# Kernel tuning notes

Hardware: AMD Instinct MI355X
Metric: run time of the kernel (lower is better)

The kernel has to match this reference:

```python
import jax, jax.numpy as jnp
import numpy as np
import math

B, H, L, S, D = 16, 10, 4096, 77, 64
N_EMB = 20            # subject tokens per instance (positions 4..23)
SHRINK = 2.0          # subj_attn_var_shrink_factor


def setup_inputs() -> dict:
    key = jax.random.key(0)
    kq, kk, kv = jax.random.split(key, 3)
    query = jax.random.normal(kq, (B, H, L, D), dtype=jnp.float32)
    k = jax.random.normal(kk, (B, H, S, D), dtype=jnp.float32)
    v = jax.random.normal(kv, (B, H, S, D), dtype=jnp.float32)
    # instance-major subject indices: every batch instance owns tokens 4..23
    idx_b = jnp.repeat(jnp.arange(B, dtype=jnp.int32), N_EMB).reshape(B, N_EMB)
    idx_n = jnp.tile(jnp.arange(4, 4 + N_EMB, dtype=jnp.int32), (B, 1))
    return {"query": query, "key": k, "value": v, "idx_b": idx_b, "idx_n": idx_n}


def _subj_attn_scales(attn_score, idx_b, idx_n, shrink_factor):
    # attn_score: [B,H,L,S] -> permute to [B,S,H,L] as in torch code
    a2 = jnp.transpose(attn_score, (0, 3, 1, 2))
    # gather subject-token attention: [N_SUB, N_EMB, H, L]
    subj = a2[idx_b, idx_n]
    n_sub, n_emb = subj.shape[0], subj.shape[1]
    subj = subj.mean(axis=2)                       # mean over heads -> [NS,NE,L]
    prob = jax.nn.softmax(subj, axis=2)            # over spatial positions
    Hs = Ws = int(math.isqrt(L))
    p3 = prob.reshape(n_sub, n_emb, Hs, Ws)        # [NS,NE,H,W]
    ys = jnp.arange(Hs, dtype=p3.dtype).reshape(1, 1, Hs, 1)
    xs = jnp.arange(Ws, dtype=p3.dtype).reshape(1, 1, 1, Ws)
    y_c = (p3 * ys).sum(axis=(2, 3))               # [NS,NE]
    x_c = (p3 * xs).sum(axis=(2, 3))
    var_y = (p3 * ys ** 2).sum(axis=(2, 3)) - y_c ** 2
    var_x = (p3 * xs ** 2).sum(axis=(2, 3)) - x_c ** 2
    s_x = jnp.sqrt(var_x) / (shrink_factor - 1.0)
    s_y = jnp.sqrt(var_y) / (shrink_factor - 1.0)
    # torch.meshgrid default is 'ij'
    X, Y = jnp.meshgrid(jnp.arange(Ws, dtype=p3.dtype), jnp.arange(Hs, dtype=p3.dtype), indexing="ij")
    X = X[:, :, None, None]
    Y = Y[:, :, None, None]
    grid = jnp.exp(-((X - x_c) ** 2 / (2 * s_x ** 2) + (Y - y_c) ** 2 / (2 * s_y ** 2)))  # [W,H,NS,NE]
    grid = grid / jax.lax.stop_gradient(grid.max())
    grid = jnp.transpose(grid, (2, 3, 0, 1)).reshape(n_sub, n_emb, 1, L)
    # scatter back into ones: [B,S,1,L]
    scales = jnp.ones((B, S, 1, L), dtype=attn_score.dtype)
    scales = scales.at[idx_b, idx_n].set(grid)
    return jnp.transpose(scales, (0, 2, 3, 1))     # [B,1,L,S]


def reference(query, key, value, idx_b, idx_n):
    scale = 1.0 / math.sqrt(query.shape[-1])
    attn_score = jnp.einsum("bhld,bhsd->bhls", query, key) * scale  # [B,H,L,S]
    scales = _subj_attn_scales(attn_score, idx_b, idx_n, SHRINK)
    attn_w = jax.nn.softmax(attn_score, axis=-1) * scales
    out = jnp.einsum("bhls,bhsd->bhld", attn_w, value)              # [B,H,L,D]
    return out
```

## Files before the change

### kernel.cpp

```cpp
#include <hip/hip_runtime.h>
#include <math.h>

#define B_ 16
#define H_ 10
#define L_ 4096
#define S_ 77
#define D_ 64
#define NE_ 20
#define NP_ (B_*NE_)
#define SHRINK_ 2.0f
#define LOG2E 1.4426950408889634f
#define SC_L2 (0.125f*LOG2E)
#define IT_ 8

typedef __bf16 bf16x8 __attribute__((ext_vector_type(8)));
typedef float  f32x4  __attribute__((ext_vector_type(4)));

static __device__ __forceinline__ unsigned short bfb(__bf16 x) {
  return __builtin_bit_cast(unsigned short, x);
}
static __device__ __forceinline__ __bf16 mkbf(unsigned short x) {
  return __builtin_bit_cast(__bf16, x);
}

__global__ __launch_bounds__(256, 3) void k1_subj(const float* __restrict__ Q,
                                                  const float* __restrict__ K,
                                                  const int* __restrict__ idxb,
                                                  const int* __restrict__ idxn,
                                                  float* __restrict__ subj) {
  __shared__ __bf16 KF[20][2][64][8];
  __shared__ float T[NE_][66];
  __shared__ int bs[NE_], ss[NE_], s_uni;
  const int i = blockIdx.y, bx = blockIdx.x;
  const int tid = threadIdx.x, lane = tid & 63, wid = tid >> 6;
  const int c = lane & 15, g = lane >> 4;
  if (tid < NE_) { bs[tid] = idxb[i*NE_ + tid]; ss[tid] = idxn[i*NE_ + tid]; }
  __syncthreads();
  if (tid == 0) { int u = 1; for (int j = 1; j < NE_; ++j) u &= (bs[j] == bs[0]); s_uni = u; }
  for (int e4 = tid; e4 < 32*160; e4 += 256) {
    int j = e4 / 160, k = (e4 - j*160) * 4;
    float4 kv = make_float4(0.f, 0.f, 0.f, 0.f);
    if (j < NE_) kv = *(const float4*)&K[(((size_t)bs[j]*H_ + (k >> 6))*S_ + ss[j])*D_ + (k & 63)];
    int ks = k >> 5, gg = (k >> 3) & 3, jj = k & 7, n = j >> 4, cc = j & 15;
    uint2 pk;
    pk.x = (unsigned)bfb((__bf16)kv.x) | ((unsigned)bfb((__bf16)kv.y) << 16);
    pk.y = (unsigned)bfb((__bf16)kv.z) | ((unsigned)bfb((__bf16)kv.w) << 16);
    *(uint2*)&KF[ks][n][gg*16 + cc][jj] = pk;
  }
  __syncthreads();
  if (!s_uni) {
    int ll = tid & 63;
    for (int ii = 0; ii < 2; ++ii) {
      int l = bx*128 + ii*64 + ll;
      for (int j = tid >> 6; j < NE_; j += 4) {
        float a = 0.f;
        for (int h = 0; h < H_; ++h) {
          const float* qp = Q + (((size_t)bs[j]*H_ + h)*L_ + l)*D_;
          const float* kp = K + (((size_t)bs[j]*H_ + h)*S_ + ss[j])*D_;
          for (int d = 0; d < 64; ++d) a += qp[d]*kp[d];
        }
        subj[(size_t)(i*NE_ + j)*L_ + l] = a * (1.0f/80.0f);
      }
    }
    return;
  }
  const int b0 = bs[0];
  #pragma unroll 1
  for (int it = 0; it < 2; ++it) {
    const int lrow = bx*128 + it*64 + wid*16 + c;
    f32x4 acc0 = {0.f,0.f,0.f,0.f}, acc1 = {0.f,0.f,0.f,0.f};
    #pragma unroll 4
    for (int ks = 0; ks < 20; ++ks) {
      const float* qp = Q + (((size_t)b0*H_ + (ks >> 1))*L_ + lrow)*D_ + (ks & 1)*32 + g*8;
      const float4 a = *(const float4*)qp;
      const float4 bq = *(const float4*)(qp + 4);
      bf16x8 af;
      af[0]=(__bf16)a.x;  af[1]=(__bf16)a.y;  af[2]=(__bf16)a.z;  af[3]=(__bf16)a.w;
      af[4]=(__bf16)bq.x; af[5]=(__bf16)bq.y; af[6]=(__bf16)bq.z; af[7]=(__bf16)bq.w;
      bf16x8 k0 = *(bf16x8*)&KF[ks][0][lane][0];
      bf16x8 k1 = *(bf16x8*)&KF[ks][1][lane][0];
      acc0 = __builtin_amdgcn_mfma_f32_16x16x32_bf16(af, k0, acc0, 0, 0, 0);
      acc1 = __builtin_amdgcn_mfma_f32_16x16x32_bf16(af, k1, acc1, 0, 0, 0);
    }
    const float sc = 1.0f/80.0f;
    #pragma unroll
    for (int r = 0; r < 4; ++r) {
      int ll = wid*16 + g*4 + r;
      T[c][ll] = acc0[r]*sc;
      if (c < 4) T[16 + c][ll] = acc1[r]*sc;
    }
    __syncthreads();
    for (int e = tid; e < NE_*64; e += 256) {
      int j = e >> 6, ll = e & 63;
      subj[(size_t)(i*NE_ + j)*L_ + bx*128 + it*64 + ll] = T[j][ll];
    }
    __syncthreads();
  }
}

__global__ __launch_bounds__(256) void k2_moments(const float* __restrict__ subj,
                                                  float* __restrict__ params) {
  const int p = blockIdx.x;
  const int tid = threadIdx.x;
  const int lane = tid & 63, wid = tid >> 6;
  const float* sp = subj + (size_t)p*L_;
  __shared__ float red[4];
  float m = -1e30f;
  for (int l = tid; l < L_; l += 256) m = fmaxf(m, sp[l]);
  #pragma unroll
  for (int s = 1; s < 64; s <<= 1) m = fmaxf(m, __shfl_xor(m, s, 64));
  if (lane == 0) red[wid] = m;
  __syncthreads();
  m = fmaxf(fmaxf(red[0], red[1]), fmaxf(red[2], red[3]));
  __syncthreads();
  float se = 0, sy = 0, sx = 0, syy = 0, sxx = 0;
  for (int l = tid; l < L_; l += 256) {
    float e = __expf(sp[l] - m);
    float y = (float)(l >> 6), x = (float)(l & 63);
    se += e; sy += e*y; sx += e*x; syy += e*y*y; sxx += e*x*x;
  }
  float vals[5] = {se, sy, sx, syy, sxx};
  #pragma unroll
  for (int q = 0; q < 5; ++q) {
    float v = vals[q];
    #pragma unroll
    for (int s = 1; s < 64; s <<= 1) v += __shfl_xor(v, s, 64);
    if (lane == 0) red[wid] = v;
    __syncthreads();
    v = red[0] + red[1] + red[2] + red[3];
    __syncthreads();
    vals[q] = v;
  }
  if (tid == 0) {
    float xc = vals[2]/vals[0], yc = vals[1]/vals[0];
    float varx = vals[4]/vals[0] - xc*xc;
    float vary = vals[3]/vals[0] - yc*yc;
    float sh = SHRINK_ - 1.0f;
    float isx = sh*sh/(2.f*varx), isy = sh*sh/(2.f*vary);
    float rx = rintf(xc), ry = rintf(yc);
    float mv = __expf(-((rx-xc)*(rx-xc)*isx + (ry-yc)*(ry-yc)*isy));
    params[p*8+0] = xc; params[p*8+1] = yc;
    params[p*8+2] = isx; params[p*8+3] = isy; params[p*8+4] = mv;
  }
}

__global__ __launch_bounds__(256) void k2b_finish(const float* __restrict__ params,
                                                  const int* __restrict__ idxb,
                                                  const int* __restrict__ idxn,
                                                  int* __restrict__ pmap,
                                                  float* __restrict__ l2invg) {
  const int tid = threadIdx.x;
  for (int e = tid; e < B_*S_; e += 256) pmap[e] = -1;
  __syncthreads();
  for (int p = tid; p < NP_; p += 256) pmap[idxb[p]*S_ + idxn[p]] = p;
  float m = 0.f;
  for (int p = tid; p < NP_; p += 256) m = fmaxf(m, params[p*8+4]);
  #pragma unroll
  for (int s = 1; s < 64; s <<= 1) m = fmaxf(m, __shfl_xor(m, s, 64));
  __shared__ float red[4];
  if ((tid & 63) == 0) red[tid >> 6] = m;
  __syncthreads();
  if (tid == 0) {
    m = fmaxf(fmaxf(red[0], red[1]), fmaxf(red[2], red[3]));
    l2invg[0] = -log2f(m);
  }
}

__global__ __launch_bounds__(256, 2) void k3_attn(const float* __restrict__ Q,
                                                  const float* __restrict__ K,
                                                  const float* __restrict__ V,
                                                  const int* __restrict__ pmap,
                                                  const float* __restrict__ params,
                                                  const float* __restrict__ l2invg,
                                                  float* __restrict__ out) {
  __shared__ __bf16 KF[2][5][64][8];
  __shared__ __bf16 VF[3][4][64][8];
  __shared__ __bf16 Wl[4][16][104];
  __shared__ float4 pp[80];
  __shared__ float  ppc[80];

  const int bh = blockIdx.y, b = bh / H_, bx = blockIdx.x;
  const int tid = threadIdx.x, lane = tid & 63, wid = tid >> 6;
  const int c = lane & 15, g = lane >> 4;

  const float* qb0 = Q + ((size_t)bh*L_ + bx*(64*IT_) + wid*16 + c)*D_ + g*8;
  float4 nqa0 = *(const float4*)(qb0);
  float4 nqa1 = *(const float4*)(qb0 + 4);
  float4 nqc0 = *(const float4*)(qb0 + 32);
  float4 nqc1 = *(const float4*)(qb0 + 36);

  *(uint2*)&Wl[wid][c][80 + g*4] = make_uint2(0u, 0u);

  for (int e4 = tid; e4 < 80*16; e4 += 256) {
    int s = e4 >> 4, d = (e4 & 15) * 4;
    float4 kv = make_float4(0.f, 0.f, 0.f, 0.f);
    if (s < S_) kv = *(const float4*)&K[((size_t)bh*S_ + s)*D_ + d];
    int n = s >> 4, cc = s & 15, ks = d >> 5, gg = (d >> 3) & 3, jj = d & 7;
    uint2 pk;
    pk.x = (unsigned)bfb((__bf16)kv.x) | ((unsigned)bfb((__bf16)kv.y) << 16);
    pk.y = (unsigned)bfb((__bf16)kv.z) | ((unsigned)bfb((__bf16)kv.w) << 16);
    *(uint2*)&KF[ks][n][gg*16 + cc][jj] = pk;
  }
  for (int e4 = tid; e4 < 96*16; e4 += 256) {
    int s = e4 >> 4, d = (e4 & 15) * 4;
    float4 vv = make_float4(0.f, 0.f, 0.f, 0.f);
    if (s < S_) vv = *(const float4*)&V[((size_t)bh*S_ + s)*D_ + d];
    int ks = s >> 5, gg = (s >> 3) & 3, jj = s & 7;
    int n0 = d >> 4, c0 = d & 15;
    VF[ks][n0][gg*16 + c0 + 0][jj] = (__bf16)vv.x;
    VF[ks][n0][gg*16 + c0 + 1][jj] = (__bf16)vv.y;
    VF[ks][n0][gg*16 + c0 + 2][jj] = (__bf16)vv.z;
    VF[ks][n0][gg*16 + c0 + 3][jj] = (__bf16)vv.w;
  }
  for (int s = tid; s < 80; s += 256) {
    float4 v = make_float4(0.f, 0.f, 0.f, 0.f);
    float cs = 0.f;
    if (s < S_) {
      int pid = pmap[b*S_ + s];
      if (pid >= 0) {
        v.x = params[pid*8+1];
        v.y = -params[pid*8+3]*LOG2E;
        v.z = params[pid*8+0];
        v.w = -params[pid*8+2]*LOG2E;
        cs  = l2invg[0];
      }
    }
    pp[s] = v; ppc[s] = cs;
  }
  __syncthreads();

  #pragma unroll 1
  for (int it = 0; it < IT_; ++it) {
    const int lt = bx*(64*IT_) + it*64 + wid*16;
    const float4 qa0 = nqa0, qa1 = nqa1, qc0 = nqc0, qc1 = nqc1;
    {
      const int itn = (it + 1 < IT_) ? it + 1 : it;
      const float* qn = qb0 + (size_t)itn * 64 * D_;
      nqa0 = *(const float4*)(qn);
      nqa1 = *(const float4*)(qn + 4);
      nqc0 = *(const float4*)(qn + 32);
      nqc1 = *(const float4*)(qn + 36);
    }

    bf16x8 qh[2], ql[2];
    {
      float vv0[8] = {qa0.x, qa0.y, qa0.z, qa0.w, qa1.x, qa1.y, qa1.z, qa1.w};
      float vv1[8] = {qc0.x, qc0.y, qc0.z, qc0.w, qc1.x, qc1.y, qc1.z, qc1.w};
      #pragma unroll
      for (int j = 0; j < 8; ++j) {
        unsigned u0 = __float_as_uint(vv0[j]);
        qh[0][j] = mkbf((unsigned short)(u0 >> 16));
        ql[0][j] = (__bf16)(vv0[j] - __uint_as_float(u0 & 0xffff0000u));
        unsigned u1 = __float_as_uint(vv1[j]);
        qh[1][j] = mkbf((unsigned short)(u1 >> 16));
        ql[1][j] = (__bf16)(vv1[j] - __uint_as_float(u1 & 0xffff0000u));
      }
    }

    f32x4 acc[5];
    #pragma unroll
    for (int n = 0; n < 5; ++n) acc[n] = f32x4{0.f, 0.f, 0.f, 0.f};
    #pragma unroll
    for (int ks = 0; ks < 2; ++ks) {
      #pragma unroll
      for (int n = 0; n < 5; ++n) {
        bf16x8 kf = *(bf16x8*)&KF[ks][n][lane][0];
        acc[n] = __builtin_amdgcn_mfma_f32_16x16x32_bf16(qh[ks], kf, acc[n], 0, 0, 0);
        acc[n] = __builtin_amdgcn_mfma_f32_16x16x32_bf16(ql[ks], kf, acc[n], 0, 0, 0);
      }
    }
    if (c >= 13) {
      #pragma unroll
      for (int r = 0; r < 4; ++r) acc[4][r] = -1e30f;
    }
    #pragma unroll
    for (int n = 0; n < 5; ++n)
      #pragma unroll
      for (int r = 0; r < 4; ++r) acc[n][r] = __builtin_amdgcn_exp2f(acc[n][r] * SC_L2);
    float sm[4];
    #pragma unroll
    for (int r = 0; r < 4; ++r) {
      float s0 = acc[0][r] + acc[1][r] + acc[2][r] + acc[3][r] + acc[4][r];
      #pragma unroll
      for (int s = 1; s < 16; s <<= 1) s0 += __shfl_xor(s0, s, 64);
      sm[r] = __builtin_amdgcn_rcpf(s0);
    }
    const float Xf = (float)(bx*IT_ + it);
    const float Yb = (float)(wid*16 + g*4);
    #pragma unroll
    for (int n = 0; n < 5; ++n) {
      const float4 sp4 = pp[16*n + c];
      const float tx = Xf - sp4.z;
      const float Cn = fmaf(tx*tx, sp4.w, ppc[16*n + c]);
      #pragma unroll
      for (int r = 0; r < 4; ++r) {
        float t = (Yb + (float)r) - sp4.x;
        float gm = __builtin_amdgcn_exp2f(fmaf(t*t, sp4.y, Cn));
        float w = acc[n][r] * gm * sm[r];
        Wl[wid][g*4 + r][16*n + c] = (__bf16)w;
      }
    }
    f32x4 pacc[4];
    #pragma unroll
    for (int n = 0; n < 4; ++n) pacc[n] = f32x4{0.f, 0.f, 0.f, 0.f};
    #pragma unroll
    for (int ks = 0; ks < 3; ++ks) {
      bf16x8 wf = *(bf16x8*)&Wl[wid][c][ks*32 + g*8];
      #pragma unroll
      for (int n = 0; n < 4; ++n) {
        bf16x8 vf = *(bf16x8*)&VF[ks][n][lane][0];
        pacc[n] = __builtin_amdgcn_mfma_f32_16x16x32_bf16(wf, vf, pacc[n], 0, 0, 0);
      }
    }
    float* ob = out + ((size_t)bh*L_ + lt + g*4)*D_ + c;
    #pragma unroll
    for (int r = 0; r < 4; ++r)
      #pragma unroll
      for (int n = 0; n < 4; ++n) ob[(size_t)r*D_ + 16*n] = pacc[n][r];
  }
}

extern "C" void kernel_launch(void* const* d_in, const int* in_sizes, int n_in,
                              void* d_out, int out_size, void* d_ws, size_t ws_size,
                              hipStream_t stream) {
  const float* Q  = (const float*)d_in[0];
  const float* Kp = (const float*)d_in[1];
  const float* Vp = (const float*)d_in[2];
  const int* idxb = (const int*)d_in[3];
  const int* idxn = (const int*)d_in[4];
  float* out = (float*)d_out;

  char* w = (char*)d_ws;
  float* params = (float*)w;
  float* l2invg = params + NP_*8;
  int* pmap = (int*)(l2invg + 4);
  size_t head = (size_t)(NP_*8 + 4)*sizeof(float) + (size_t)B_*S_*sizeof(int);
  head = (head + 255) & ~(size_t)255;
  float* subj;
  if (ws_size >= head + (size_t)NP_*L_*sizeof(float))
    subj = (float*)(w + head);
  else
    subj = out;

  k1_subj<<<dim3(L_/128, B_), 256, 0, stream>>>(Q, Kp, idxb, idxn, subj);
  k2_moments<<<NP_, 256, 0, stream>>>(subj, params);
  k2b_finish<<<1, 256, 0, stream>>>(params, idxb, idxn, pmap, l2invg);
  k3_attn<<<dim3(L_/(64*IT_), B_*H_), 256, 0, stream>>>(Q, Kp, Vp, pmap, params, l2invg, out);
}
```

Baseline: 132.6 us.

## Drop split-bf16 Q, cache K/V fragments in registers, halve tile iterations

```diff
diff --git a/kernel.cpp b/kernel.cpp
--- a/kernel.cpp
+++ b/kernel.cpp
@@ -11,7 +11,7 @@
 #define SHRINK_ 2.0f
 #define LOG2E 1.4426950408889634f
 #define SC_L2 (0.125f*LOG2E)
-#define IT_ 8
+#define IT_ 4
 
 typedef __bf16 bf16x8 __attribute__((ext_vector_type(8)));
 typedef float  f32x4  __attribute__((ext_vector_type(4)));
@@ -166,7 +166,7 @@
   }
 }
 
-__global__ __launch_bounds__(256, 2) void k3_attn(const float* __restrict__ Q,
+__global__ __launch_bounds__(256, 1) void k3_attn(const float* __restrict__ Q,
                                                   const float* __restrict__ K,
                                                   const float* __restrict__ V,
                                                   const int* __restrict__ pmap,
@@ -229,6 +229,16 @@
   }
   __syncthreads();
 
+  bf16x8 kfr[2][5], vfr[3][4];
+  #pragma unroll
+  for (int ks = 0; ks < 2; ++ks)
+    #pragma unroll
+    for (int n = 0; n < 5; ++n) kfr[ks][n] = *(bf16x8*)&KF[ks][n][lane][0];
+  #pragma unroll
+  for (int ks = 0; ks < 3; ++ks)
+    #pragma unroll
+    for (int n = 0; n < 4; ++n) vfr[ks][n] = *(bf16x8*)&VF[ks][n][lane][0];
+
   #pragma unroll 1
   for (int it = 0; it < IT_; ++it) {
     const int lt = bx*(64*IT_) + it*64 + wid*16;
@@ -241,34 +251,20 @@
       nqc0 = *(const float4*)(qn + 32);
       nqc1 = *(const float4*)(qn + 36);
     }
-
-    bf16x8 qh[2], ql[2];
-    {
-      float vv0[8] = {qa0.x, qa0.y, qa0.z, qa0.w, qa1.x, qa1.y, qa1.z, qa1.w};
-      float vv1[8] = {qc0.x, qc0.y, qc0.z, qc0.w, qc1.x, qc1.y, qc1.z, qc1.w};
-      #pragma unroll
-      for (int j = 0; j < 8; ++j) {
-        unsigned u0 = __float_as_uint(vv0[j]);
-        qh[0][j] = mkbf((unsigned short)(u0 >> 16));
-        ql[0][j] = (__bf16)(vv0[j] - __uint_as_float(u0 & 0xffff0000u));
-        unsigned u1 = __float_as_uint(vv1[j]);
-        qh[1][j] = mkbf((unsigned short)(u1 >> 16));
-        ql[1][j] = (__bf16)(vv1[j] - __uint_as_float(u1 & 0xffff0000u));
-      }
-    }
+    bf16x8 qf[2];
+    qf[0][0]=(__bf16)qa0.x; qf[0][1]=(__bf16)qa0.y; qf[0][2]=(__bf16)qa0.z; qf[0][3]=(__bf16)qa0.w;
+    qf[0][4]=(__bf16)qa1.x; qf[0][5]=(__bf16)qa1.y; qf[0][6]=(__bf16)qa1.z; qf[0][7]=(__bf16)qa1.w;
+    qf[1][0]=(__bf16)qc0.x; qf[1][1]=(__bf16)qc0.y; qf[1][2]=(__bf16)qc0.z; qf[1][3]=(__bf16)qc0.w;
+    qf[1][4]=(__bf16)qc1.x; qf[1][5]=(__bf16)qc1.y; qf[1][6]=(__bf16)qc1.z; qf[1][7]=(__bf16)qc1.w;
 
     f32x4 acc[5];
     #pragma unroll
     for (int n = 0; n < 5; ++n) acc[n] = f32x4{0.f, 0.f, 0.f, 0.f};
     #pragma unroll
-    for (int ks = 0; ks < 2; ++ks) {
-      #pragma unroll
-      for (int n = 0; n < 5; ++n) {
-        bf16x8 kf = *(bf16x8*)&KF[ks][n][lane][0];
-        acc[n] = __builtin_amdgcn_mfma_f32_16x16x32_bf16(qh[ks], kf, acc[n], 0, 0, 0);
-        acc[n] = __builtin_amdgcn_mfma_f32_16x16x32_bf16(ql[ks], kf, acc[n], 0, 0, 0);
-      }
-    }
+    for (int ks = 0; ks < 2; ++ks)
+      #pragma unroll
+      for (int n = 0; n < 5; ++n)
+        acc[n] = __builtin_amdgcn_mfma_f32_16x16x32_bf16(qf[ks], kfr[ks][n], acc[n], 0, 0, 0);
     if (c >= 13) {
       #pragma unroll
       for (int r = 0; r < 4; ++r) acc[4][r] = -1e30f;
@@ -307,10 +303,8 @@
     for (int ks = 0; ks < 3; ++ks) {
       bf16x8 wf = *(bf16x8*)&Wl[wid][c][ks*32 + g*8];
       #pragma unroll
-      for (int n = 0; n < 4; ++n) {
-        bf16x8 vf = *(bf16x8*)&VF[ks][n][lane][0];
-        pacc[n] = __builtin_amdgcn_mfma_f32_16x16x32_bf16(wf, vf, pacc[n], 0, 0, 0);
-      }
+      for (int n = 0; n < 4; ++n)
+        pacc[n] = __builtin_amdgcn_mfma_f32_16x16x32_bf16(wf, vfr[ks][n], pacc[n], 0, 0, 0);
     }
     float* ob = out + ((size_t)bh*L_ + lt + g*4)*D_ + c;
     #pragma unroll
```

Measured after the change: 139.1 us. +5.0%, slower.
